# Kernel optimization log

Measured on AMD Instinct MI355X. Metric: run time of the kernel, lower is better.

The kernel has to match this reference:

```python
import jax, jax.numpy as jnp
import numpy as np

FEATURE_MAPS = [38, 19, 10, 5, 3, 1]
NUM_ANCHORS = [4, 6, 6, 6, 4, 4]
SCALE_RANGE = (0.1, 0.9)
RATIO_RANGE = (0.5, 2.0)
BACKGROUND_ID = 0
EPS = 1e-6


def make_anchors():
    # Replicates AnchorManager._generate_anchors: for each level, loop i (rows -> cy),
    # j (cols -> cx), then zip(scales, ratios) anchor shapes. Returns [A, 4] cxcywh.
    all_a = []
    for size, na in zip(FEATURE_MAPS, NUM_ANCHORS):
        scales = np.linspace(SCALE_RANGE[0], SCALE_RANGE[1], na)
        ratios = np.linspace(RATIO_RANGE[0], RATIO_RANGE[1], na)
        rs = np.sqrt(ratios)
        w = scales * rs
        h = scales / rs
        c = (np.arange(size) + 0.5) / size
        cy_g, cx_g = np.meshgrid(c, c, indexing='ij')  # i -> cy, j -> cx
        centers = np.stack([cx_g.ravel(), cy_g.ravel()], axis=-1)  # [size*size, 2]
        wh = np.stack([w, h], axis=-1)  # [na, 2]
        a = np.concatenate([np.repeat(centers, na, axis=0), np.tile(wh, (size * size, 1))], axis=1)
        all_a.append(a)
    return np.concatenate(all_a).astype(np.float32)  # [8732, 4]


def _cxcywh_to_xyxy(b):
    return jnp.concatenate([b[..., :2] - b[..., 2:] * 0.5, b[..., :2] + b[..., 2:] * 0.5], axis=-1)


def _pairwise_iou(a, b):
    # a: [B, A, 4] xyxy, b: [B, N, 4] xyxy -> [B, A, N]
    lt = jnp.maximum(a[:, :, None, :2], b[:, None, :, :2])
    rb = jnp.minimum(a[:, :, None, 2:], b[:, None, :, 2:])
    wh = jnp.clip(rb - lt, 0.0)
    inter = wh[..., 0] * wh[..., 1]
    area_a = (a[..., 2] - a[..., 0]) * (a[..., 3] - a[..., 1])
    area_b = (b[..., 2] - b[..., 0]) * (b[..., 3] - b[..., 1])
    union = area_a[:, :, None] + area_b[:, None, :] - inter
    return inter / jnp.maximum(union, EPS)


def setup_inputs() -> dict:
    key = jax.random.key(0)
    k1, k2 = jax.random.split(key)
    B, N = 32, 100
    gt_boxes = jax.random.uniform(k1, (B, N, 4), dtype=jnp.float32)
    gt_labels = jax.random.randint(k2, (B, N), 0, 81, dtype=jnp.int32)
    mask = jnp.ones((B, N), dtype=bool)
    anchors = jnp.asarray(make_anchors())
    return {"gt_boxes": gt_boxes, "gt_labels": gt_labels, "mask": mask, "anchors": anchors}


def reference(gt_boxes, gt_labels, mask, anchors):
    B, N, _ = gt_boxes.shape
    A = anchors.shape[0]
    anc = jnp.broadcast_to(anchors, (B, A, 4))
    anc_xyxy = _cxcywh_to_xyxy(anc)
    ious = _pairwise_iou(anc_xyxy, gt_boxes)  # [B, A, N]

    best_gt_iou = ious.max(axis=-1)          # [B, A]
    best_gt_idx = ious.argmax(axis=-1)       # [B, A]
    best_anchor_idx = ious.argmax(axis=-2)   # [B, N]

    bidx = jnp.arange(B)[:, None]
    best_gt_idx = best_gt_idx.at[bidx, best_anchor_idx].set(jnp.broadcast_to(jnp.arange(N), (B, N)))
    best_gt_iou = best_gt_iou.at[bidx, best_anchor_idx].set(2.0)

    pos_mask = best_gt_iou > 0.5  # [B, A]

    matched_gtb = jnp.take_along_axis(gt_boxes, best_gt_idx[..., None], axis=1)  # [B, A, 4]
    matched_lab = jnp.take_along_axis(gt_labels, best_gt_idx, axis=1)           # [B, A]

    ex = (matched_gtb[..., 0] - anc[..., 0]) / anc[..., 2]
    ey = (matched_gtb[..., 1] - anc[..., 1]) / anc[..., 3]
    ew = jnp.log((matched_gtb[..., 2] + EPS) / (anc[..., 2] + EPS))
    eh = jnp.log((matched_gtb[..., 3] + EPS) / (anc[..., 3] + EPS))
    encoded = jnp.stack([ex, ey, ew, eh], axis=-1)  # [B, A, 4]

    encoded_labels = jnp.where(pos_mask, matched_lab, jnp.int32(BACKGROUND_ID))

    # Batches with no valid GT keep zeros / background (the `continue` branch)
    any_valid = mask.any(axis=-1)  # [B]
    encoded = jnp.where(any_valid[:, None, None], encoded, 0.0)
    encoded_labels = jnp.where(any_valid[:, None], encoded_labels, jnp.int32(BACKGROUND_ID))
    return encoded, encoded_labels, pos_mask
```

## Files before the change

### kernel.cpp

```cpp
#include <hip/hip_runtime.h>

#define A_ 8732
#define B_ 32
#define N_ 100
#define ABLK 35
#define GB_G 4
#define GMAX 25
#define SPLIT 8
#define SLEN 1092
#define EPSF 1e-6f



__global__ __launch_bounds__(256) void k_scan(
    const float* __restrict__ gt, const float* __restrict__ anchors,
    unsigned long long* __restrict__ partial,
    unsigned long long* __restrict__ wsplit) {
  int tid = threadIdx.x;
  int lane = tid & 63, wid = tid >> 6;
  int bid = blockIdx.x;
  int s = bid % SPLIT;
  int t = bid / SPLIT;
  int g = t % GMAX;
  int b = t / GMAX;

  __shared__ unsigned long long s_bal[2];
  __shared__ int s_slot[N_];
  __shared__ unsigned long long s_w[4][GB_G];

  bool v = false;
  float4 myg;
  if (tid < N_) {
    myg = ((const float4*)gt)[b * N_ + tid];
    v = (myg.z > myg.x && myg.w > myg.y);
  }
  unsigned long long bal = __ballot(v);
  if (lane == 0 && wid < 2) s_bal[wid] = bal;
  __syncthreads();
  int c0 = __popcll(s_bal[0]);
  int c = c0 + __popcll(s_bal[1]);
  if (v) {
    int rank = __popcll(bal & ((1ull << lane) - 1)) + (wid ? c0 : 0);
    s_slot[rank] = tid;
  }
  __syncthreads();
  if (GB_G * g >= c) return;

  float gx0[GB_G], gy0[GB_G], gx1[GB_G], gy1[GB_G], gar[GB_G];
  int gn[GB_G];
  bool live[GB_G];
#pragma unroll
  for (int j = 0; j < GB_G; j++) {
    int p = GB_G * g + j;
    live[j] = p < c;
    int nj = live[j] ? s_slot[p] : 0;
    gn[j] = nj;
    float4 gb = ((const float4*)gt)[b * N_ + nj];
    if (!live[j]) gb = make_float4(1.0f, 1.0f, 0.0f, 0.0f);
    gx0[j] = gb.x; gy0[j] = gb.y; gx1[j] = gb.z; gy1[j] = gb.w;
    gar[j] = (gb.z - gb.x) * (gb.w - gb.y);
  }

  int s0 = s * SLEN;
  int send = (s0 + SLEN < A_) ? (s0 + SLEN) : A_;

  unsigned long long wkey[GB_G];
#pragma unroll
  for (int j = 0; j < GB_G; j++)
    wkey[j] = (unsigned long long)(0xFFFFFFFFu - (unsigned)(s0 + tid));

  unsigned long long* prow = partial + ((size_t)b * GMAX + g) * A_;
  for (int a = s0 + tid; a < send; a += 256) {
    float4 an = ((const float4*)anchors)[a];
    float ax0 = an.x - an.z * 0.5f, ay0 = an.y - an.w * 0.5f;
    float ax1 = an.x + an.z * 0.5f, ay1 = an.y + an.w * 0.5f;
    float area_a = (ax1 - ax0) * (ay1 - ay0);
    unsigned long long pk = 0ull;
#pragma unroll
    for (int j = 0; j < GB_G; j++) {
      float lx = fmaxf(ax0, gx0[j]), ly = fmaxf(ay0, gy0[j]);
      float rx = fminf(ax1, gx1[j]), ry = fminf(ay1, gy1[j]);
      float w = fmaxf(rx - lx, 0.0f), h = fmaxf(ry - ly, 0.0f);
      float inter = w * h;
      if (inter > 0.0f) {
        float uni = area_a + gar[j] - inter;
        float iou = inter / fmaxf(uni, EPSF);
        unsigned long long hi = ((unsigned long long)__float_as_uint(iou)) << 32;
        unsigned long long kA = hi | (unsigned long long)(unsigned)(N_ - 1 - gn[j]);
        if (kA > pk) pk = kA;
        unsigned long long kB = hi | (unsigned long long)(0xFFFFFFFFu - (unsigned)a);
        if (kB > wkey[j]) wkey[j] = kB;
      }
    }
    prow[a] = pk;
  }

#pragma unroll
  for (int j = 0; j < GB_G; j++) {
    unsigned long long k = wkey[j];
#pragma unroll
    for (int off = 32; off; off >>= 1) {
      unsigned long long o = __shfl_xor(k, off, 64);
      if (o > k) k = o;
    }
    if (lane == 0) s_w[wid][j] = k;
  }
  __syncthreads();
  if (tid < GB_G) {
    int j = tid;
    if (GB_G * g + j < c) {
      unsigned long long k = s_w[0][j];
#pragma unroll
      for (int w2 = 1; w2 < 4; w2++)
        if (s_w[w2][j] > k) k = s_w[w2][j];
      wsplit[((size_t)b * SPLIT + s) * N_ + s_slot[GB_G * g + j]] = k;
    }
  }
}

__global__ __launch_bounds__(256) void k_finalize(
    const float* __restrict__ gt, const int* __restrict__ labels,
    const float* __restrict__ anchors, const unsigned char* __restrict__ mask,
    const unsigned long long* __restrict__ partial,
    const unsigned long long* __restrict__ wsplit, float* __restrict__ out) {
  int b = blockIdx.y;
  int a0 = blockIdx.x * 256;
  int tid = threadIdx.x;
  int lane = tid & 63, wid = tid >> 6;
  int a = a0 + tid;

  __shared__ int s_ov[256];
  __shared__ int s_any;
  __shared__ unsigned long long s_bal[2];

  bool v = false;
  if (tid < N_) {
    float4 gb = ((const float4*)gt)[b * N_ + tid];
    v = (gb.z > gb.x && gb.w > gb.y);
  }
  unsigned long long bal = __ballot(v);
  if (lane == 0 && wid < 2) s_bal[wid] = bal;
  if (tid == 0) s_any = 0;
  s_ov[tid] = -1;
  __syncthreads();
  int c = __popcll(s_bal[0]) + __popcll(s_bal[1]);

  if (tid < N_) {
    int aw = 0;
    if (v) {
      const unsigned long long* wp = wsplit + (size_t)b * SPLIT * N_ + tid;
      unsigned long long k = wp[0];
#pragma unroll
      for (int s2 = 1; s2 < SPLIT; s2++) {
        unsigned long long tk = wp[(size_t)s2 * N_];
        if (tk > k) k = tk;
      }
      aw = (int)(0xFFFFFFFFu - (unsigned)(k & 0xFFFFFFFFull));
    }
    if (aw >= a0 && aw < a0 + 256) atomicMax(&s_ov[aw - a0], tid);
  }
  if (tid < 25) {
    unsigned mv = ((const unsigned*)mask)[b * 25 + tid];
    if (mv) atomicOr(&s_any, 1);
  }
  __syncthreads();
  if (a >= A_) return;

  int G = (c + GB_G - 1) / GB_G;
  unsigned long long k = (unsigned long long)(unsigned)(N_ - 1);
  const unsigned long long* prow = partial + (size_t)b * GMAX * A_ + a;
  for (int g2 = 0; g2 < G; g2++) {
    unsigned long long t2 = prow[(size_t)g2 * A_];
    if (t2 > k) k = t2;
  }
  float iou = __uint_as_float((unsigned)(k >> 32));
  int gi = (N_ - 1) - (int)(k & 0xFFFFFFFFull);

  int ov = s_ov[tid];
  bool pos;
  if (ov >= 0) {
    gi = ov;
    pos = true;
  } else {
    pos = iou > 0.5f;
  }

  float4 an = ((const float4*)anchors)[a];
  const float* g = gt + (size_t)(b * N_ + gi) * 4;
  float gx = g[0], gy = g[1], gw = g[2], gh = g[3];

  float ex = (gx - an.x) / an.z;
  float ey = (gy - an.y) / an.w;
  float ew = logf((gw + EPSF) / (an.z + EPSF));
  float eh = logf((gh + EPSF) / (an.w + EPSF));
  int lab = pos ? labels[b * N_ + gi] : 0;

  if (!s_any) { ex = 0.0f; ey = 0.0f; ew = 0.0f; eh = 0.0f; lab = 0; }

  const long long BA = (long long)B_ * A_;
  ((float4*)out)[(size_t)b * A_ + a] = make_float4(ex, ey, ew, eh);
  out[4 * BA + (size_t)b * A_ + a] = (float)lab;
  out[5 * BA + (size_t)b * A_ + a] = pos ? 1.0f : 0.0f;
}

extern "C" void kernel_launch(void* const* d_in, const int* in_sizes, int n_in,
                              void* d_out, int out_size, void* d_ws,
                              size_t ws_size, hipStream_t stream) {
  const float* gt = (const float*)d_in[0];
  const int* labels = (const int*)d_in[1];
  const unsigned char* mask = (const unsigned char*)d_in[2];
  const float* anchors = (const float*)d_in[3];
  float* out = (float*)d_out;

  unsigned long long* partial = (unsigned long long*)d_ws;
  unsigned long long* wsplit = partial + (size_t)B_ * GMAX * A_;

  k_scan<<<B_ * GMAX * SPLIT, 256, 0, stream>>>(gt, anchors, partial, wsplit);
  k_finalize<<<dim3(ABLK, B_), 256, 0, stream>>>(gt, labels, anchors, mask,
                                                 partial, wsplit, out);
}
```

Before: 83.24 us.

## Tile scan by anchor blocks, loop all GTs per block to drop partial buffer

The scan kernel changes from one block per (batch, GT group, anchor split) to one block per (batch, 256-anchor tile). Each thread keeps its anchor in registers and loops over all valid GTs staged in shared memory, so it writes a single best-GT key per anchor. This removes the large per-group partial buffer and the multi-row reduction in finalize. In exchange, each block runs a serial GT loop with two barriers per group of four GTs, launches far fewer blocks, and finalize now reduces per-GT keys over 35 tiles instead of 8 splits.

```diff
diff --git a/kernel.cpp b/kernel.cpp
--- a/kernel.cpp
+++ b/kernel.cpp
@@ -3,30 +3,26 @@
 #define A_ 8732
 #define B_ 32
 #define N_ 100
-#define ABLK 35
-#define GB_G 4
-#define GMAX 25
-#define SPLIT 8
-#define SLEN 1092
+#define NT 35
+#define GB 4
 #define EPSF 1e-6f
-
 
 
 __global__ __launch_bounds__(256) void k_scan(
     const float* __restrict__ gt, const float* __restrict__ anchors,
-    unsigned long long* __restrict__ partial,
+    unsigned long long* __restrict__ pbest,
     unsigned long long* __restrict__ wsplit) {
   int tid = threadIdx.x;
   int lane = tid & 63, wid = tid >> 6;
-  int bid = blockIdx.x;
-  int s = bid % SPLIT;
-  int t = bid / SPLIT;
-  int g = t % GMAX;
-  int b = t / GMAX;
+  int t = blockIdx.x, b = blockIdx.y;
+  int a0 = t * 256;
+  int a = a0 + tid;
 
   __shared__ unsigned long long s_bal[2];
-  __shared__ int s_slot[N_];
-  __shared__ unsigned long long s_w[4][GB_G];
+  __shared__ float4 s_cgt[N_];
+  __shared__ float s_gar[N_];
+  __shared__ int s_cn[N_];
+  __shared__ unsigned long long s_w[4][GB];
 
   bool v = false;
   float4 myg;
@@ -36,48 +32,53 @@
   }
   unsigned long long bal = __ballot(v);
   if (lane == 0 && wid < 2) s_bal[wid] = bal;
-  __syncthreads();
+
+  float ax0 = 2.0f, ay0 = 2.0f, ax1 = 2.0f, ay1 = 2.0f, area_a = 0.0f;
+  if (a < A_) {
+    float4 an = ((const float4*)anchors)[a];
+    ax0 = an.x - an.z * 0.5f;
+    ay0 = an.y - an.w * 0.5f;
+    ax1 = an.x + an.z * 0.5f;
+    ay1 = an.y + an.w * 0.5f;
+    area_a = (ax1 - ax0) * (ay1 - ay0);
+  }
+  __syncthreads();
+
   int c0 = __popcll(s_bal[0]);
   int c = c0 + __popcll(s_bal[1]);
-  if (v) {
-    int rank = __popcll(bal & ((1ull << lane) - 1)) + (wid ? c0 : 0);
-    s_slot[rank] = tid;
-  }
-  __syncthreads();
-  if (GB_G * g >= c) return;
-
-  float gx0[GB_G], gy0[GB_G], gx1[GB_G], gy1[GB_G], gar[GB_G];
-  int gn[GB_G];
-  bool live[GB_G];
-#pragma unroll
-  for (int j = 0; j < GB_G; j++) {
-    int p = GB_G * g + j;
-    live[j] = p < c;
-    int nj = live[j] ? s_slot[p] : 0;
-    gn[j] = nj;
-    float4 gb = ((const float4*)gt)[b * N_ + nj];
-    if (!live[j]) gb = make_float4(1.0f, 1.0f, 0.0f, 0.0f);
-    gx0[j] = gb.x; gy0[j] = gb.y; gx1[j] = gb.z; gy1[j] = gb.w;
-    gar[j] = (gb.z - gb.x) * (gb.w - gb.y);
-  }
-
-  int s0 = s * SLEN;
-  int send = (s0 + SLEN < A_) ? (s0 + SLEN) : A_;
-
-  unsigned long long wkey[GB_G];
-#pragma unroll
-  for (int j = 0; j < GB_G; j++)
-    wkey[j] = (unsigned long long)(0xFFFFFFFFu - (unsigned)(s0 + tid));
-
-  unsigned long long* prow = partial + ((size_t)b * GMAX + g) * A_;
-  for (int a = s0 + tid; a < send; a += 256) {
-    float4 an = ((const float4*)anchors)[a];
-    float ax0 = an.x - an.z * 0.5f, ay0 = an.y - an.w * 0.5f;
-    float ax1 = an.x + an.z * 0.5f, ay1 = an.y + an.w * 0.5f;
-    float area_a = (ax1 - ax0) * (ay1 - ay0);
-    unsigned long long pk = 0ull;
-#pragma unroll
-    for (int j = 0; j < GB_G; j++) {
+  if (tid < N_) {
+    if (v) {
+      int rank = __popcll(bal & ((1ull << lane) - 1)) + (wid ? c0 : 0);
+      s_cgt[rank] = myg;
+      s_gar[rank] = (myg.z - myg.x) * (myg.w - myg.y);
+      s_cn[rank] = tid;
+    } else {
+      wsplit[((size_t)b * NT + t) * N_ + tid] =
+          (unsigned long long)(0xFFFFFFFFu - (unsigned)a0);
+    }
+  }
+  __syncthreads();
+
+  unsigned long long ak = (unsigned long long)(unsigned)(N_ - 1);
+  unsigned kinvA = 0xFFFFFFFFu - (unsigned)a;
+
+  for (int pc = 0; pc < c; pc += GB) {
+    float gx0[GB], gy0[GB], gx1[GB], gy1[GB], gar[GB];
+#pragma unroll
+    for (int j = 0; j < GB; j++) {
+      int p = pc + j;
+      bool live = p < c;
+      float4 gb = live ? s_cgt[p] : make_float4(1.0f, 1.0f, 0.0f, 0.0f);
+      gx0[j] = gb.x; gy0[j] = gb.y; gx1[j] = gb.z; gy1[j] = gb.w;
+      gar[j] = live ? s_gar[p] : 0.0f;
+    }
+
+    unsigned long long wk[GB];
+#pragma unroll
+    for (int j = 0; j < GB; j++) wk[j] = (unsigned long long)kinvA;
+
+#pragma unroll
+    for (int j = 0; j < GB; j++) {
       float lx = fmaxf(ax0, gx0[j]), ly = fmaxf(ay0, gy0[j]);
       float rx = fminf(ax1, gx1[j]), ry = fminf(ay1, gy1[j]);
       float w = fmaxf(rx - lx, 0.0f), h = fmaxf(ry - ly, 0.0f);
@@ -86,77 +87,66 @@
         float uni = area_a + gar[j] - inter;
         float iou = inter / fmaxf(uni, EPSF);
         unsigned long long hi = ((unsigned long long)__float_as_uint(iou)) << 32;
-        unsigned long long kA = hi | (unsigned long long)(unsigned)(N_ - 1 - gn[j]);
-        if (kA > pk) pk = kA;
-        unsigned long long kB = hi | (unsigned long long)(0xFFFFFFFFu - (unsigned)a);
-        if (kB > wkey[j]) wkey[j] = kB;
+        int p = pc + j;
+        int nj = (p < c) ? s_cn[p] : 0;
+        unsigned long long kA =
+            hi | (unsigned long long)(unsigned)(N_ - 1 - nj);
+        if (kA > ak) ak = kA;
+        unsigned long long kB = hi | (unsigned long long)kinvA;
+        if (kB > wk[j]) wk[j] = kB;
       }
     }
-    prow[a] = pk;
-  }
-
-#pragma unroll
-  for (int j = 0; j < GB_G; j++) {
-    unsigned long long k = wkey[j];
-#pragma unroll
-    for (int off = 32; off; off >>= 1) {
-      unsigned long long o = __shfl_xor(k, off, 64);
-      if (o > k) k = o;
-    }
-    if (lane == 0) s_w[wid][j] = k;
-  }
-  __syncthreads();
-  if (tid < GB_G) {
-    int j = tid;
-    if (GB_G * g + j < c) {
-      unsigned long long k = s_w[0][j];
+
+#pragma unroll
+    for (int j = 0; j < GB; j++) {
+      unsigned long long k = wk[j];
+#pragma unroll
+      for (int off = 32; off; off >>= 1) {
+        unsigned long long o = __shfl_xor(k, off, 64);
+        if (o > k) k = o;
+      }
+      if (lane == 0) s_w[wid][j] = k;
+    }
+    __syncthreads();
+    if (tid < GB && pc + tid < c) {
+      unsigned long long k = s_w[0][tid];
 #pragma unroll
       for (int w2 = 1; w2 < 4; w2++)
-        if (s_w[w2][j] > k) k = s_w[w2][j];
-      wsplit[((size_t)b * SPLIT + s) * N_ + s_slot[GB_G * g + j]] = k;
-    }
-  }
+        if (s_w[w2][tid] > k) k = s_w[w2][tid];
+      wsplit[((size_t)b * NT + t) * N_ + s_cn[pc + tid]] = k;
+    }
+    __syncthreads();
+  }
+
+  if (a < A_) pbest[(size_t)b * A_ + a] = ak;
 }
 
 __global__ __launch_bounds__(256) void k_finalize(
     const float* __restrict__ gt, const int* __restrict__ labels,
     const float* __restrict__ anchors, const unsigned char* __restrict__ mask,
-    const unsigned long long* __restrict__ partial,
+    const unsigned long long* __restrict__ pbest,
     const unsigned long long* __restrict__ wsplit, float* __restrict__ out) {
   int b = blockIdx.y;
   int a0 = blockIdx.x * 256;
   int tid = threadIdx.x;
-  int lane = tid & 63, wid = tid >> 6;
   int a = a0 + tid;
 
   __shared__ int s_ov[256];
   __shared__ int s_any;
-  __shared__ unsigned long long s_bal[2];
-
-  bool v = false;
-  if (tid < N_) {
-    float4 gb = ((const float4*)gt)[b * N_ + tid];
-    v = (gb.z > gb.x && gb.w > gb.y);
-  }
-  unsigned long long bal = __ballot(v);
-  if (lane == 0 && wid < 2) s_bal[wid] = bal;
+
   if (tid == 0) s_any = 0;
   s_ov[tid] = -1;
   __syncthreads();
-  int c = __popcll(s_bal[0]) + __popcll(s_bal[1]);
 
   if (tid < N_) {
-    int aw = 0;
-    if (v) {
-      const unsigned long long* wp = wsplit + (size_t)b * SPLIT * N_ + tid;
-      unsigned long long k = wp[0];
-#pragma unroll
-      for (int s2 = 1; s2 < SPLIT; s2++) {
-        unsigned long long tk = wp[(size_t)s2 * N_];
-        if (tk > k) k = tk;
-      }
-      aw = (int)(0xFFFFFFFFu - (unsigned)(k & 0xFFFFFFFFull));
-    }
+    const unsigned long long* wp = wsplit + (size_t)b * NT * N_ + tid;
+    unsigned long long k = wp[0];
+#pragma unroll
+    for (int t2 = 1; t2 < NT; t2++) {
+      unsigned long long tk = wp[(size_t)t2 * N_];
+      if (tk > k) k = tk;
+    }
+    int aw = (int)(0xFFFFFFFFu - (unsigned)(k & 0xFFFFFFFFull));
     if (aw >= a0 && aw < a0 + 256) atomicMax(&s_ov[aw - a0], tid);
   }
   if (tid < 25) {
@@ -166,13 +156,7 @@
   __syncthreads();
   if (a >= A_) return;
 
-  int G = (c + GB_G - 1) / GB_G;
-  unsigned long long k = (unsigned long long)(unsigned)(N_ - 1);
-  const unsigned long long* prow = partial + (size_t)b * GMAX * A_ + a;
-  for (int g2 = 0; g2 < G; g2++) {
-    unsigned long long t2 = prow[(size_t)g2 * A_];
-    if (t2 > k) k = t2;
-  }
+  unsigned long long k = pbest[(size_t)b * A_ + a];
   float iou = __uint_as_float((unsigned)(k >> 32));
   int gi = (N_ - 1) - (int)(k & 0xFFFFFFFFull);
 
@@ -212,10 +196,10 @@
   const float* anchors = (const float*)d_in[3];
   float* out = (float*)d_out;
 
-  unsigned long long* partial = (unsigned long long*)d_ws;
-  unsigned long long* wsplit = partial + (size_t)B_ * GMAX * A_;
-
-  k_scan<<<B_ * GMAX * SPLIT, 256, 0, stream>>>(gt, anchors, partial, wsplit);
-  k_finalize<<<dim3(ABLK, B_), 256, 0, stream>>>(gt, labels, anchors, mask,
-                                                 partial, wsplit, out);
+  unsigned long long* pbest = (unsigned long long*)d_ws;
+  unsigned long long* wsplit = pbest + (size_t)B_ * A_;
+
+  k_scan<<<dim3(NT, B_), 256, 0, stream>>>(gt, anchors, pbest, wsplit);
+  k_finalize<<<dim3(NT, B_), 256, 0, stream>>>(gt, labels, anchors, mask,
+                                               pbest, wsplit, out);
 }
```

After: 93.50 us. 12.3% more time.
